# Optimization experiments

Measured on AMD Instinct MI355X. Metric: run time of the kernel, lower is better.

The kernel has to match this reference:

```python
import jax, jax.numpy as jnp
import numpy as np

B_BATCH = 16384   # number of independent control queries (timesteps/trials)
P = 32            # observation dim p = C.shape[0]
MC = 16           # control dim m_control = B.shape[1]
H = 24            # h (== h_tilde in the module, since it sets self.h_tilde = h)
M = 64            # m (== m_tilde, since the module sets self.m_tilde = m)
L = M + M + 1     # history length needed: max delay is j+k = m_tilde + m - 1


def setup_inputs() -> dict:
    key = jax.random.key(0)
    ks = jax.random.split(key, 9)
    return {
        # y_rev[b, d, :] == y_nat_history[-d-1] (most-recent-first reversed history)
        "y_rev": jax.random.normal(ks[0], (B_BATCH, L, P), dtype=jnp.float32),
        "M0": jax.random.normal(ks[1], (MC, P), dtype=jnp.float32),
        "M_tilde": jax.random.normal(ks[2], (H, MC, P), dtype=jnp.float32),
        "M_0l": jax.random.normal(ks[3], (H, MC, P), dtype=jnp.float32),
        "M_big": jax.random.normal(ks[4], (H, H, MC, P), dtype=jnp.float32),
        # eigenvalues of the PSD Hankel matrices: positive
        "sigma": jax.random.uniform(ks[5], (H,), dtype=jnp.float32, minval=0.01, maxval=1.0),
        "lambda_e": jax.random.uniform(ks[6], (H,), dtype=jnp.float32, minval=0.01, maxval=1.0),
        "phi": jax.random.normal(ks[7], (M, H), dtype=jnp.float32),
        "phi_tilde": jax.random.normal(ks[8], (M, H), dtype=jnp.float32),
    }


def reference(y_rev, M0, M_tilde, M_0l, M_big, sigma, lambda_e, phi, phi_tilde):
    # Term 1: M_0 @ y_t  -> [B, MC]
    u = jnp.einsum("cp,bp->bc", M0, y_rev[:, 0])

    # Term 2: sum_{i,j>=1} lambda_i^{1/4} phi_tilde[j-1,i] (M_tilde[i] @ y_{t-j})
    pt = phi_tilde * (lambda_e ** 0.25)[None, :]            # [M, H] (j-1, i)
    T2 = jnp.einsum("ji,icp->jcp", pt, M_tilde)             # [M, MC, P]
    u = u + jnp.einsum("jcp,bjp->bc", T2, y_rev[:, 1:M + 1])

    # Term 3: sum_{l,k>=0} sigma_l^{1/4} phi[k,l] (M_0l[l] @ y_{t-k})
    ps = phi * (sigma ** 0.25)[None, :]                     # [M, H] (k, l)
    T3 = jnp.einsum("kl,lcp->kcp", ps, M_0l)                # [M, MC, P]
    u = u + jnp.einsum("kcp,bkp->bc", T3, y_rev[:, 0:M])

    # Term 4: sum_{i,j,l,k} (sigma_l lambda_i)^{1/4} phi[k,l] phi_tilde[j-1,i] (M[i][l] @ y_{t-j-k})
    # Collapse (j,k) into delay d=j+k via 1-D convolution per (i,l):
    #   conv(phi_tilde[:,i], phi[:,l])[n] corresponds to delay d = n+1.
    conv = jax.vmap(jax.vmap(jnp.convolve, in_axes=(None, 1)), in_axes=(1, None))
    W4 = conv(phi_tilde, phi)                               # [H(i), H(l), 2M-1]
    scale = (lambda_e[:, None] * sigma[None, :]) ** 0.25    # [H(i), H(l)]
    T4 = jnp.einsum("ild,ilcp->dcp", W4 * scale[:, :, None], M_big)  # [2M-1, MC, P]
    u = u + jnp.einsum("dcp,bdp->bc", T4, y_rev[:, 1:2 * M])

    return u  # [B, MC]
```

## Files before the change

kernel.cpp:

```cpp
#include <hip/hip_runtime.h>

#define BB    16384
#define PP    32
#define MCC   16
#define HH    24
#define MM    64
#define LL    129
#define YROW  (LL*PP)
#define KK    (128*PP)

#define ROWS   64
#define TPB    512
#define STAGES 32
#define SK     128
#define BUFF   (ROWS*SK/4)

__device__ __forceinline__ float rl(float v, int lane) {
    return __int_as_float(__builtin_amdgcn_readlane(__float_as_int(v), lane));
}

__global__ __launch_bounds__(256) void setup_k(
    const float* __restrict__ M0,  const float* __restrict__ Mt,
    const float* __restrict__ M0l, const float* __restrict__ Mb,
    const float* __restrict__ sig, const float* __restrict__ lam,
    const float* __restrict__ phi, const float* __restrict__ phit,
    float* __restrict__ Wk)
{
    __shared__ float sA[MM*HH];
    __shared__ float sB[MM*HH];
    __shared__ float sWd[HH*HH];

    const int t = threadIdx.x;
    const int d = blockIdx.x >> 1;
    const int h = blockIdx.x & 1;

#pragma unroll
    for (int r = 0; r < 6; ++r) {
        int e = t + r*256;
        int col = e % HH;
        sA[e] = phit[e] * sqrtf(sqrtf(lam[col]));
        sB[e] = phi[e]  * sqrtf(sqrtf(sig[col]));
    }
    __syncthreads();

    if (d >= 1) {
        const int n  = d - 1;
        const int lo = n > 63 ? n - 63 : 0;
        const int hi = n < 63 ? n : 63;
        for (int e = t; e < HH*HH; e += 256) {
            int i = e / HH, l = e % HH;
            float s = 0.f;
            for (int j = lo; j <= hi; ++j) s += sA[j*HH + i] * sB[(n - j)*HH + l];
            sWd[e] = s;
        }
    }
    __syncthreads();

    const int c = h*8 + (t >> 5);
    const int p = t & 31;
    float wv = 0.f;
    if (d == 0) wv += M0[c*PP + p];
    if (d >= 1 && d <= MM) {
        const int j = d - 1;
#pragma unroll
        for (int i = 0; i < HH; ++i) wv += sA[j*HH + i] * Mt[(i*MCC + c)*PP + p];
    }
    if (d < MM) {
#pragma unroll
        for (int l = 0; l < HH; ++l) wv += sB[d*HH + l] * M0l[(l*MCC + c)*PP + p];
    }
    if (d >= 1) {
        const float* mb = Mb + h*256 + t;
#pragma unroll 16
        for (int e = 0; e < HH*HH; ++e) wv += sWd[e] * mb[e*512];
    }
    Wk[(d*PP + p)*MCC + c] = wv;
}

#define FMASTEP(YV, J)                                                       \
    acc[0]  = fmaf(rl(Wc.x, (J)     ), (YV), acc[0]);                        \
    acc[1]  = fmaf(rl(Wc.y, (J)     ), (YV), acc[1]);                        \
    acc[2]  = fmaf(rl(Wc.z, (J)     ), (YV), acc[2]);                        \
    acc[3]  = fmaf(rl(Wc.w, (J)     ), (YV), acc[3]);                        \
    acc[4]  = fmaf(rl(Wc.x, (J) + 16), (YV), acc[4]);                        \
    acc[5]  = fmaf(rl(Wc.y, (J) + 16), (YV), acc[5]);                        \
    acc[6]  = fmaf(rl(Wc.z, (J) + 16), (YV), acc[6]);                        \
    acc[7]  = fmaf(rl(Wc.w, (J) + 16), (YV), acc[7]);                        \
    acc[8]  = fmaf(rl(Wc.x, (J) + 32), (YV), acc[8]);                        \
    acc[9]  = fmaf(rl(Wc.y, (J) + 32), (YV), acc[9]);                        \
    acc[10] = fmaf(rl(Wc.z, (J) + 32), (YV), acc[10]);                       \
    acc[11] = fmaf(rl(Wc.w, (J) + 32), (YV), acc[11]);                       \
    acc[12] = fmaf(rl(Wc.x, (J) + 48), (YV), acc[12]);                       \
    acc[13] = fmaf(rl(Wc.y, (J) + 48), (YV), acc[13]);                       \
    acc[14] = fmaf(rl(Wc.z, (J) + 48), (YV), acc[14]);                       \
    acc[15] = fmaf(rl(Wc.w, (J) + 48), (YV), acc[15]);

__global__ __launch_bounds__(512) void main_k(
    const float* __restrict__ Y, const float* __restrict__ Wk,
    float* __restrict__ out)
{
    __shared__ float4 sY[2*BUFF];

    const int t    = threadIdx.x;
    const int w    = t >> 6;
    const int lane = t & 63;
    const int blk  = blockIdx.x;

    const int srow = t >> 3, kq = t & 7;
    const float* yst = Y + (size_t)(blk*ROWS + srow)*YROW + kq*16;
    const int wx = srow*32;
    const int sx = srow & 7;

    const int rbase4 = lane*32;
    const int rx     = lane & 7;

    const float* wst = Wk + ((w*16 + (lane & 15))*MCC + (lane >> 4)*4);

    float acc[16];
#pragma unroll
    for (int c = 0; c < 16; ++c) acc[c] = 0.f;

    float4 Yr[4], Wn, Wc;
#pragma unroll
    for (int i = 0; i < 4; ++i) Yr[i] = *(const float4*)(yst + 4*i);
    Wn = *(const float4*)(wst);
#pragma unroll
    for (int i = 0; i < 4; ++i)
        sY[wx + ((kq*4 + i) ^ sx)] = Yr[i];

#pragma unroll 1
    for (int s = 0; s < STAGES; ++s) {
        const int cur = s & 1;

        Wc = Wn;
        if (s < STAGES - 1) {
            const float* yp = yst + (s + 1)*SK;
#pragma unroll
            for (int i = 0; i < 4; ++i) Yr[i] = *(const float4*)(yp + 4*i);
            Wn = *(const float4*)(wst + (size_t)(s + 1)*SK*MCC);
        }

        __syncthreads();

        const float4* yb = &sY[cur*BUFF];
#pragma unroll
        for (int j4 = 0; j4 < 4; ++j4) {
            float4 y4 = yb[rbase4 + ((w*4 + j4) ^ rx)];
            FMASTEP(y4.x, j4*4 + 0)
            FMASTEP(y4.y, j4*4 + 1)
            FMASTEP(y4.z, j4*4 + 2)
            FMASTEP(y4.w, j4*4 + 3)
        }

        if (s < STAGES - 1) {
            float4* ob = &sY[(cur ^ 1)*BUFF];
#pragma unroll
            for (int i = 0; i < 4; ++i)
                ob[wx + ((kq*4 + i) ^ sx)] = Yr[i];
        }
    }

    __syncthreads();
    float* red = (float*)sY;
#pragma unroll
    for (int c = 0; c < 16; ++c) red[t*16 + c] = acc[c];
    __syncthreads();

    if (t < 256) {
        const int row = t >> 2, c4 = t & 3;
        float4 sum = make_float4(0.f, 0.f, 0.f, 0.f);
#pragma unroll
        for (int ww = 0; ww < 8; ++ww) {
            const float* rp = &red[(ww*64 + row)*16 + c4*4];
            sum.x += rp[0]; sum.y += rp[1]; sum.z += rp[2]; sum.w += rp[3];
        }
        *(float4*)(out + (size_t)(blk*ROWS + row)*MCC + c4*4) = sum;
    }
}

extern "C" void kernel_launch(void* const* d_in, const int* in_sizes, int n_in,
                              void* d_out, int out_size, void* d_ws, size_t ws_size,
                              hipStream_t stream) {
    (void)in_sizes; (void)n_in; (void)out_size; (void)ws_size;
    const float* y    = (const float*)d_in[0];
    const float* M0   = (const float*)d_in[1];
    const float* Mt   = (const float*)d_in[2];
    const float* M0l  = (const float*)d_in[3];
    const float* Mb   = (const float*)d_in[4];
    const float* sig  = (const float*)d_in[5];
    const float* lam  = (const float*)d_in[6];
    const float* phi  = (const float*)d_in[7];
    const float* phit = (const float*)d_in[8];

    float* Wk  = (float*)d_ws;
    float* out = (float*)d_out;

    setup_k<<<256, 256, 0, stream>>>(M0, Mt, M0l, Mb, sig, lam, phi, phit, Wk);
    main_k<<<256, TPB, 0, stream>>>(y, Wk, out);
}
```

Before: 472.0 us.

## Use direct global-to-LDS async loads with manual vmcnt pipelining in main kernel

Replaces the register-staged Y loads (global to VGPR, then LDS store) with global_load_lds DMA straight into a double-buffered shared tile. The stage loop is unrolled by two, with explicit s_waitcnt vmcnt and raw s_barrier calls, so the next stage's data arrives while the current one computes. The swizzle moves to the global source addresses so the LDS layout matches the reader's XOR pattern. The reduction scratch uses a stride of 17 to avoid LDS bank conflicts. The hand-tuned vmcnt count is fragile: if the compiler issues a different number of outstanding loads, the code could read stale data.

```diff
diff --git a/kernel.cpp b/kernel.cpp
--- a/kernel.cpp
+++ b/kernel.cpp
@@ -13,10 +13,16 @@
 #define TPB    512
 #define STAGES 32
 #define SK     128
-#define BUFF   (ROWS*SK/4)
+#define BUF4   2048
 
 __device__ __forceinline__ float rl(float v, int lane) {
     return __int_as_float(__builtin_amdgcn_readlane(__float_as_int(v), lane));
+}
+
+__device__ __forceinline__ void dma16(const float* g, float4* l) {
+    __builtin_amdgcn_global_load_lds(
+        (const __attribute__((address_space(1))) void*)g,
+        (__attribute__((address_space(3))) void*)l, 16, 0, 0);
 }
 
 __global__ __launch_bounds__(256) void setup_k(
@@ -77,93 +83,118 @@
     Wk[(d*PP + p)*MCC + c] = wv;
 }
 
-#define FMASTEP(YV, J)                                                       \
-    acc[0]  = fmaf(rl(Wc.x, (J)     ), (YV), acc[0]);                        \
-    acc[1]  = fmaf(rl(Wc.y, (J)     ), (YV), acc[1]);                        \
-    acc[2]  = fmaf(rl(Wc.z, (J)     ), (YV), acc[2]);                        \
-    acc[3]  = fmaf(rl(Wc.w, (J)     ), (YV), acc[3]);                        \
-    acc[4]  = fmaf(rl(Wc.x, (J) + 16), (YV), acc[4]);                        \
-    acc[5]  = fmaf(rl(Wc.y, (J) + 16), (YV), acc[5]);                        \
-    acc[6]  = fmaf(rl(Wc.z, (J) + 16), (YV), acc[6]);                        \
-    acc[7]  = fmaf(rl(Wc.w, (J) + 16), (YV), acc[7]);                        \
-    acc[8]  = fmaf(rl(Wc.x, (J) + 32), (YV), acc[8]);                        \
-    acc[9]  = fmaf(rl(Wc.y, (J) + 32), (YV), acc[9]);                        \
-    acc[10] = fmaf(rl(Wc.z, (J) + 32), (YV), acc[10]);                       \
-    acc[11] = fmaf(rl(Wc.w, (J) + 32), (YV), acc[11]);                       \
-    acc[12] = fmaf(rl(Wc.x, (J) + 48), (YV), acc[12]);                       \
-    acc[13] = fmaf(rl(Wc.y, (J) + 48), (YV), acc[13]);                       \
-    acc[14] = fmaf(rl(Wc.z, (J) + 48), (YV), acc[14]);                       \
-    acc[15] = fmaf(rl(Wc.w, (J) + 48), (YV), acc[15]);
+#define FMASTEP(WV, YV, J)                                              \
+    acc[0]  = fmaf(rl((WV).x, (J)     ), (YV), acc[0]);                 \
+    acc[1]  = fmaf(rl((WV).y, (J)     ), (YV), acc[1]);                 \
+    acc[2]  = fmaf(rl((WV).z, (J)     ), (YV), acc[2]);                 \
+    acc[3]  = fmaf(rl((WV).w, (J)     ), (YV), acc[3]);                 \
+    acc[4]  = fmaf(rl((WV).x, (J) + 16), (YV), acc[4]);                 \
+    acc[5]  = fmaf(rl((WV).y, (J) + 16), (YV), acc[5]);                 \
+    acc[6]  = fmaf(rl((WV).z, (J) + 16), (YV), acc[6]);                 \
+    acc[7]  = fmaf(rl((WV).w, (J) + 16), (YV), acc[7]);                 \
+    acc[8]  = fmaf(rl((WV).x, (J) + 32), (YV), acc[8]);                 \
+    acc[9]  = fmaf(rl((WV).y, (J) + 32), (YV), acc[9]);                 \
+    acc[10] = fmaf(rl((WV).z, (J) + 32), (YV), acc[10]);                \
+    acc[11] = fmaf(rl((WV).w, (J) + 32), (YV), acc[11]);                \
+    acc[12] = fmaf(rl((WV).x, (J) + 48), (YV), acc[12]);                \
+    acc[13] = fmaf(rl((WV).y, (J) + 48), (YV), acc[13]);                \
+    acc[14] = fmaf(rl((WV).z, (J) + 48), (YV), acc[14]);                \
+    acc[15] = fmaf(rl((WV).w, (J) + 48), (YV), acc[15]);
+
+#define STAGE_COMPUTE(YB, WV)                                           \
+    {                                                                   \
+        float4 y0 = (YB)[rbase + ((w4 + 0) ^ rx)];                      \
+        float4 y1 = (YB)[rbase + ((w4 + 1) ^ rx)];                      \
+        float4 y2 = (YB)[rbase + ((w4 + 2) ^ rx)];                      \
+        float4 y3 = (YB)[rbase + ((w4 + 3) ^ rx)];                      \
+        FMASTEP(WV, y0.x, 0)  FMASTEP(WV, y0.y, 1)                      \
+        FMASTEP(WV, y0.z, 2)  FMASTEP(WV, y0.w, 3)                      \
+        FMASTEP(WV, y1.x, 4)  FMASTEP(WV, y1.y, 5)                      \
+        FMASTEP(WV, y1.z, 6)  FMASTEP(WV, y1.w, 7)                      \
+        FMASTEP(WV, y2.x, 8)  FMASTEP(WV, y2.y, 9)                      \
+        FMASTEP(WV, y2.z, 10) FMASTEP(WV, y2.w, 11)                     \
+        FMASTEP(WV, y3.x, 12) FMASTEP(WV, y3.y, 13)                     \
+        FMASTEP(WV, y3.z, 14) FMASTEP(WV, y3.w, 15)                     \
+    }
 
 __global__ __launch_bounds__(512) void main_k(
     const float* __restrict__ Y, const float* __restrict__ Wk,
     float* __restrict__ out)
 {
-    __shared__ float4 sY[2*BUFF];
+    __shared__ float4 sY[2*BUF4];
 
     const int t    = threadIdx.x;
     const int w    = t >> 6;
     const int lane = t & 63;
     const int blk  = blockIdx.x;
 
-    const int srow = t >> 3, kq = t & 7;
-    const float* yst = Y + (size_t)(blk*ROWS + srow)*YROW + kq*16;
-    const int wx = srow*32;
-    const int sx = srow & 7;
-
-    const int rbase4 = lane*32;
-    const int rx     = lane & 7;
-
-    const float* wst = Wk + ((w*16 + (lane & 15))*MCC + (lane >> 4)*4);
+    const float* gsrc[4];
+#pragma unroll
+    for (int i = 0; i < 4; ++i) {
+        const int row = w*8 + i*2 + (lane >> 5);
+        const int col = (lane & 31) ^ (row & 7);
+        gsrc[i] = Y + (size_t)(blk*ROWS + row)*YROW + col*4;
+    }
+    float4* const d0 = &sY[        w*256];
+    float4* const d1 = &sY[BUF4 + w*256];
+
+    const int w4    = w*4;
+    const int rbase = lane*32;
+    const int rx    = lane & 7;
+
+    const float* wsrc = Wk + ((w*16 + (lane & 15))*MCC + (lane >> 4)*4);
 
     float acc[16];
 #pragma unroll
     for (int c = 0; c < 16; ++c) acc[c] = 0.f;
 
-    float4 Yr[4], Wn, Wc;
-#pragma unroll
-    for (int i = 0; i < 4; ++i) Yr[i] = *(const float4*)(yst + 4*i);
-    Wn = *(const float4*)(wst);
-#pragma unroll
-    for (int i = 0; i < 4; ++i)
-        sY[wx + ((kq*4 + i) ^ sx)] = Yr[i];
+    float4 Wa, Wb;
+    const float4* buf0 = sY;
+    const float4* buf1 = sY + BUF4;
+
+    Wa = *(const float4*)(wsrc);
+#pragma unroll
+    for (int i = 0; i < 4; ++i) dma16(gsrc[i],      d0 + i*64);
+    Wb = *(const float4*)(wsrc + SK*MCC);
+#pragma unroll
+    for (int i = 0; i < 4; ++i) dma16(gsrc[i] + SK, d1 + i*64);
 
 #pragma unroll 1
-    for (int s = 0; s < STAGES; ++s) {
-        const int cur = s & 1;
-
-        Wc = Wn;
-        if (s < STAGES - 1) {
-            const float* yp = yst + (s + 1)*SK;
-#pragma unroll
-            for (int i = 0; i < 4; ++i) Yr[i] = *(const float4*)(yp + 4*i);
-            Wn = *(const float4*)(wst + (size_t)(s + 1)*SK*MCC);
-        }
-
-        __syncthreads();
-
-        const float4* yb = &sY[cur*BUFF];
-#pragma unroll
-        for (int j4 = 0; j4 < 4; ++j4) {
-            float4 y4 = yb[rbase4 + ((w*4 + j4) ^ rx)];
-            FMASTEP(y4.x, j4*4 + 0)
-            FMASTEP(y4.y, j4*4 + 1)
-            FMASTEP(y4.z, j4*4 + 2)
-            FMASTEP(y4.w, j4*4 + 3)
-        }
-
-        if (s < STAGES - 1) {
-            float4* ob = &sY[(cur ^ 1)*BUFF];
-#pragma unroll
-            for (int i = 0; i < 4; ++i)
-                ob[wx + ((kq*4 + i) ^ sx)] = Yr[i];
+    for (int sp = 0; sp < 16; ++sp) {
+        asm volatile("s_waitcnt vmcnt(5)" ::: "memory");
+        __builtin_amdgcn_s_barrier();
+        asm volatile("" ::: "memory");
+        STAGE_COMPUTE(buf0, Wa)
+        asm volatile("" ::: "memory");
+        __builtin_amdgcn_s_barrier();
+        asm volatile("" ::: "memory");
+        if (sp < 15) {
+            const int sn = 2*sp + 2;
+            Wa = *(const float4*)(wsrc + (size_t)sn*SK*MCC);
+#pragma unroll
+            for (int i = 0; i < 4; ++i) dma16(gsrc[i] + sn*SK, d0 + i*64);
+        }
+
+        if (sp == 15) asm volatile("s_waitcnt vmcnt(0)" ::: "memory");
+        else          asm volatile("s_waitcnt vmcnt(5)" ::: "memory");
+        __builtin_amdgcn_s_barrier();
+        asm volatile("" ::: "memory");
+        STAGE_COMPUTE(buf1, Wb)
+        asm volatile("" ::: "memory");
+        __builtin_amdgcn_s_barrier();
+        asm volatile("" ::: "memory");
+        if (sp < 15) {
+            const int sn = 2*sp + 3;
+            Wb = *(const float4*)(wsrc + (size_t)sn*SK*MCC);
+#pragma unroll
+            for (int i = 0; i < 4; ++i) dma16(gsrc[i] + sn*SK, d1 + i*64);
         }
     }
 
     __syncthreads();
     float* red = (float*)sY;
 #pragma unroll
-    for (int c = 0; c < 16; ++c) red[t*16 + c] = acc[c];
+    for (int c = 0; c < 16; ++c) red[t*17 + c] = acc[c];
     __syncthreads();
 
     if (t < 256) {
@@ -171,7 +202,7 @@
         float4 sum = make_float4(0.f, 0.f, 0.f, 0.f);
 #pragma unroll
         for (int ww = 0; ww < 8; ++ww) {
-            const float* rp = &red[(ww*64 + row)*16 + c4*4];
+            const float* rp = &red[(ww*64 + row)*17 + c4*4];
             sum.x += rp[0]; sum.y += rp[1]; sum.z += rp[2]; sum.w += rp[3];
         }
         *(float4*)(out + (size_t)(blk*ROWS + row)*MCC + c4*4) = sum;
```

Measured after the change: 461.6 us. -2.2%, faster.
